# Optimization experiments

Measured on AMD Instinct MI355X. Metric: run time of the kernel, lower is better.

Reference implementation:

```python
import jax, jax.numpy as jnp
import numpy as np

N_NODES = 50000
N_EDGES = 200000
D = 128
LN_EPS = 1e-5


def _layer_norm(x, g, b):
    mu = jnp.mean(x, axis=-1, keepdims=True)
    var = jnp.mean(jnp.square(x - mu), axis=-1, keepdims=True)
    return (x - mu) * jax.lax.rsqrt(var + LN_EPS) * g + b


def _mlp(x, W1, b1, W2, b2, W3, b3, g, beta):
    # 2 hidden ReLU layers + linear output + LayerNorm (MeshGraphNets style)
    h = jax.nn.relu(x @ W1 + b1)
    h = jax.nn.relu(h @ W2 + b2)
    h = h @ W3 + b3
    return _layer_norm(h, g, beta)


def setup_inputs() -> dict:
    key = jax.random.key(0)
    ks = jax.random.split(key, 12)
    d = {}
    d["node_features"] = jax.random.normal(ks[0], (N_NODES, D), dtype=jnp.float32)
    d["edge_features"] = jax.random.normal(ks[1], (N_EDGES, D), dtype=jnp.float32)
    d["senders"] = jax.random.randint(ks[2], (N_EDGES,), 0, N_NODES, dtype=jnp.int32)
    d["receivers"] = jax.random.randint(ks[3], (N_EDGES,), 0, N_NODES, dtype=jnp.int32)
    def lin(k, fan_in, fan_out):
        return jax.random.normal(k, (fan_in, fan_out), dtype=jnp.float32) / np.sqrt(fan_in)
    # edge MLP: [3D] -> D -> D -> D
    d["We1"] = lin(ks[4], 3 * D, D); d["be1"] = jnp.zeros((D,), jnp.float32)
    d["We2"] = lin(ks[5], D, D);     d["be2"] = jnp.zeros((D,), jnp.float32)
    d["We3"] = lin(ks[6], D, D);     d["be3"] = jnp.zeros((D,), jnp.float32)
    d["ge"] = jnp.ones((D,), jnp.float32); d["bege"] = jnp.zeros((D,), jnp.float32)
    # node MLP: [2D] -> D -> D -> D
    d["Wn1"] = lin(ks[7], 2 * D, D); d["bn1"] = jnp.zeros((D,), jnp.float32)
    d["Wn2"] = lin(ks[8], D, D);     d["bn2"] = jnp.zeros((D,), jnp.float32)
    d["Wn3"] = lin(ks[9], D, D);     d["bn3"] = jnp.zeros((D,), jnp.float32)
    d["gn"] = jnp.ones((D,), jnp.float32); d["begn"] = jnp.zeros((D,), jnp.float32)
    return d


def reference(node_features, edge_features, senders, receivers,
              We1, be1, We2, be2, We3, be3, ge, bege,
              Wn1, bn1, Wn2, bn2, Wn3, bn3, gn, begn):
    num_nodes = node_features.shape[0]
    # --- edge update: gather sender/receiver feats, concat, edge MLP ---
    edge_in = jnp.concatenate(
        [node_features[senders], node_features[receivers], edge_features], axis=-1)  # [E, 3D]
    new_edge = _mlp(edge_in, We1, be1, We2, be2, We3, be3, ge, bege)  # [E, D]
    # --- node update: scatter-sum aggregate, concat, node MLP ---
    agg = jax.ops.segment_sum(new_edge, receivers, num_segments=num_nodes)  # [N, D]
    node_in = jnp.concatenate([node_features, agg], axis=-1)  # [N, 2D]
    new_node = _mlp(node_in, Wn1, bn1, Wn2, bn2, Wn3, bn3, gn, begn)
    # --- residuals ---
    new_node = new_node + node_features
    new_edge = new_edge + edge_features
    return new_node, new_edge
```

## Files before the change

kernel.cpp:

```cpp
#include <hip/hip_runtime.h>

#define NNODES 50000
#define NEDGES 200000
#define DD 128
#define LN_EPS 1e-5f
#define NTH 256

typedef __attribute__((ext_vector_type(8))) short bf16x8;
typedef __attribute__((ext_vector_type(4))) float f32x4;
typedef __attribute__((ext_vector_type(16))) float f32x16;

template<int N> struct ic { static constexpr int value = N; };

__device__ __forceinline__ unsigned short bfr(float f) {
    union { float f; unsigned u; } v; v.f = f;
    return (unsigned short)((v.u + 0x7fffu + ((v.u >> 16) & 1u)) >> 16);
}
__device__ __forceinline__ unsigned pk2(float a, float b) {
    return (unsigned)bfr(a) | ((unsigned)bfr(b) << 16);
}
__device__ __forceinline__ void gload_lds16(const void* g, void* l) {
    __builtin_amdgcn_global_load_lds(
        (const __attribute__((address_space(1))) void*)g,
        (__attribute__((address_space(3))) void*)l, 16, 0, 0);
}

__global__ __launch_bounds__(NTH)
void prepass(const float* __restrict__ We1, const float* __restrict__ We2,
             const float* __restrict__ We3, const float* __restrict__ Wn1,
             const float* __restrict__ Wn2, const float* __restrict__ Wn3,
             char* __restrict__ img_e, char* __restrict__ img_n,
             const float* __restrict__ nodef, const int* __restrict__ recv,
             uint4* __restrict__ nodb, int* __restrict__ cnt) {
    if (blockIdx.x < 72) {
        int tid = blockIdx.x * NTH + threadIdx.x;
        const float* W; char* dst; int q;
        if      (tid <  6144) { W = We1; dst = img_e;             q = tid;         }
        else if (tid <  8192) { W = We2; dst = img_e + 12 * 8192; q = tid - 6144;  }
        else if (tid < 10240) { W = We3; dst = img_e + 16 * 8192; q = tid - 8192;  }
        else if (tid < 14336) { W = Wn1; dst = img_n;             q = tid - 10240; }
        else if (tid < 16384) { W = Wn2; dst = img_n + 8 * 8192;  q = tid - 14336; }
        else if (tid < 18432) { W = Wn3; dst = img_n + 12 * 8192; q = tid - 16384; }
        else return;
        int c = q >> 9, rem = q & 511;
        int nt = rem >> 7, r2 = rem & 127, n32 = r2 >> 2, ks = r2 & 3;
        int n = nt * 32 + n32;
        int sx = (n32 + (n32 >> 2)) & 3;
        int k0 = c * 32 + ks * 8;
        unsigned short o[8];
        #pragma unroll
        for (int e = 0; e < 8; ++e)
            o[e] = bfr(W[(size_t)(k0 + e) * DD + n]);
        uint4 val;
        val.x = (unsigned)o[0] | ((unsigned)o[1] << 16);
        val.y = (unsigned)o[2] | ((unsigned)o[3] << 16);
        val.z = (unsigned)o[4] | ((unsigned)o[5] << 16);
        val.w = (unsigned)o[6] | ((unsigned)o[7] << 16);
        *(uint4*)(dst + (size_t)c * 8192 + nt * 2048 + n32 * 64 + ((ks ^ sx) << 4)) = val;
    } else {
        const int b = blockIdx.x - 72;
        const int tid0 = b * NTH + threadIdx.x;
        if (tid0 < NEDGES) atomicAdd(&cnt[recv[tid0]], 1);
        const int NG = NNODES * 16;
        for (int g = tid0; g < NG; g += 1024 * NTH) {
            f32x4 a = ((const f32x4*)nodef)[g * 2];
            f32x4 bb = ((const f32x4*)nodef)[g * 2 + 1];
            uint4 o;
            o.x = pk2(a[0], a[1]); o.y = pk2(a[2], a[3]);
            o.z = pk2(bb[0], bb[1]); o.w = pk2(bb[2], bb[3]);
            nodb[g] = o;
        }
    }
}

__global__ __launch_bounds__(NTH)
void csr_scan1(const int* __restrict__ cnt, int* __restrict__ part) {
    __shared__ int red[NTH];
    const int b = blockIdx.x, t = threadIdx.x;
    const int base = b * 196;
    int s = 0;
    for (int i = t; i < 196; i += NTH) {
        int idx = base + i;
        if (idx < NNODES) s += cnt[idx];
    }
    red[t] = s;
    __syncthreads();
    for (int d = NTH / 2; d > 0; d >>= 1) {
        if (t < d) red[t] += red[t + d];
        __syncthreads();
    }
    if (t == 0) part[b] = red[0];
}

__global__ __launch_bounds__(NTH)
void csr_scan2(const int* __restrict__ cnt, const int* __restrict__ part,
               int* __restrict__ off, int* __restrict__ cursor) {
    __shared__ int sp[NTH];
    const int t = threadIdx.x;
    sp[t] = part[t];
    __syncthreads();
    for (int d = 1; d < NTH; d <<= 1) {
        int v = (t >= d) ? sp[t - d] : 0;
        __syncthreads();
        sp[t] += v;
        __syncthreads();
    }
    int run = (t == 0) ? 0 : sp[t - 1];
    const int base = t * 196;
    for (int i = 0; i < 196; ++i) {
        int idx = base + i;
        if (idx < NNODES) { off[idx] = run; cursor[idx] = run; run += cnt[idx]; }
    }
    if (t == NTH - 1) off[NNODES] = NEDGES;
}

__global__ __launch_bounds__(NTH)
void aggregate(const unsigned* __restrict__ ybuf,
               const int* __restrict__ off,
               unsigned* __restrict__ aggb) {
    const int n = blockIdx.x * 4 + (threadIdx.x >> 6);
    const int l = threadIdx.x & 63;
    if (n >= NNODES) return;
    const int j0 = off[n], j1 = off[n + 1];
    float sx = 0.f, sy = 0.f;
    int j = j0;
    for (; j + 4 <= j1; j += 4) {
        unsigned v0 = ybuf[(size_t)j * 64 + l];
        unsigned v1 = ybuf[(size_t)(j + 1) * 64 + l];
        unsigned v2 = ybuf[(size_t)(j + 2) * 64 + l];
        unsigned v3 = ybuf[(size_t)(j + 3) * 64 + l];
        sx += __uint_as_float(v0 << 16) + __uint_as_float(v1 << 16)
            + __uint_as_float(v2 << 16) + __uint_as_float(v3 << 16);
        sy += __uint_as_float(v0 & 0xffff0000u) + __uint_as_float(v1 & 0xffff0000u)
            + __uint_as_float(v2 & 0xffff0000u) + __uint_as_float(v3 & 0xffff0000u);
    }
    for (; j < j1; ++j) {
        unsigned v = ybuf[(size_t)j * 64 + l];
        sx += __uint_as_float(v << 16);
        sy += __uint_as_float(v & 0xffff0000u);
    }
    aggb[(size_t)n * 64 + l] = pk2(sx, sy);
}

template<int MODE>
__global__ __launch_bounds__(NTH, 2)
void mgn_mfma(const float* __restrict__ nodef, const float* __restrict__ edgef,
              const unsigned short* __restrict__ nodb,
              const int* __restrict__ senders, const int* __restrict__ receivers,
              int* __restrict__ cursor,
              const char* __restrict__ img,
              const float* __restrict__ b1, const float* __restrict__ b2,
              const float* __restrict__ b3,
              const float* __restrict__ gamma, const float* __restrict__ beta,
              const unsigned short* __restrict__ aggb, unsigned* __restrict__ ybuf,
              float* __restrict__ outp)
{
    __shared__ char Wbuf[6 * 8192];
    __shared__ char Hb[4 * 8192];

    const int t  = threadIdx.x;
    const int w  = t >> 6;
    const int l  = t & 63;
    const int ln = l & 31;
    const int hi = l >> 5;
    const int row0 = blockIdx.x * 128;
    const int gm = row0 + w * 32 + ln;
    constexpr int NROWS = (MODE == 0) ? NEDGES : NNODES;
    constexpr int NK1   = (MODE == 0) ? 12 : 8;
    constexpr int NCH   = NK1 + 8;
    const int gmc = gm < NROWS ? gm : NROWS - 1;
    const int sxA = (ln + (ln >> 2)) & 3;
    const int sxH = ln & 15;

    int srow = 0, rrow = 0, prow = 0;
    if (MODE == 0) {
        srow = senders[gmc]; rrow = receivers[gmc];
        int pclaim = 0;
        if (hi == 0 && gm < NROWS) pclaim = atomicAdd(&cursor[rrow], 1);
        prow = __shfl(pclaim, ln);
    }

    const f32x16 fz = {0.f,0.f,0.f,0.f,0.f,0.f,0.f,0.f,
                       0.f,0.f,0.f,0.f,0.f,0.f,0.f,0.f};
    f32x16 acc[4];
    #pragma unroll
    for (int nt = 0; nt < 4; ++nt) acc[nt] = fz;

    bf16x8 bS[4][2];
    f32x4  fS[4][4];

    auto stageW = [&](int c) {
        const char* src = img + (size_t)c * 8192 + t * 16;
        char* dstl = Wbuf + (c % 6) * 8192 + t * 16;
        gload_lds16(src, dstl);
        gload_lds16(src + 4096, dstl + 4096);
    };

    auto loadBB = [&](auto CC, bf16x8* dst) {
        constexpr int c = decltype(CC)::value;
        const unsigned short* base;
        if constexpr (MODE == 0) {
            base = (c < 4) ? nodb + (size_t)srow * DD : nodb + (size_t)rrow * DD;
        } else {
            base = (c < 4) ? nodb + (size_t)gmc * DD : aggb + (size_t)gmc * DD;
        }
        const char* p = (const char*)base + (c & 3) * 64 + hi * 16;
        dst[0] = *(const bf16x8*)p;
        dst[1] = *(const bf16x8*)(p + 32);
    };

    auto loadBF = [&](auto CC, f32x4* dst) {
        constexpr int c = decltype(CC)::value;
        const float* p = edgef + (size_t)gmc * DD + (c & 3) * 32 + hi * 8;
        dst[0] = *(const f32x4*)p;
        dst[1] = *(const f32x4*)(p + 4);
        dst[2] = *(const f32x4*)(p + 16);
        dst[3] = *(const f32x4*)(p + 20);
    };

    auto cvtB = [&](const f32x4* br) {
        union { unsigned u[4]; bf16x8 v; } r;
        r.u[0] = pk2(br[0][0], br[0][1]);
        r.u[1] = pk2(br[0][2], br[0][3]);
        r.u[2] = pk2(br[1][0], br[1][1]);
        r.u[3] = pk2(br[1][2], br[1][3]);
        return r.v;
    };

    auto loadBH = [&](int ks, int kh) {
        const char* p = Hb + w * 8192 + ln * 256
                      + (((ks * 4 + kh * 2 + hi) ^ sxH) << 4);
        return *(const bf16x8*)p;
    };

    auto getB = [&](auto CC, int kh) -> bf16x8 {
        constexpr int c = decltype(CC)::value;
        if constexpr (c >= NK1) {
            return loadBH((c - NK1) & 3, kh);
        } else if constexpr (MODE == 0 && c >= 8) {
            return cvtB(&fS[c & 3][kh * 2]);
        } else {
            return bS[c & 3][kh];
        }
    };

    auto compute = [&](auto CC) {
        constexpr int c = decltype(CC)::value;
        const char* bp = Wbuf + (c % 6) * 8192 + ln * 64;
        #pragma unroll
        for (int kh = 0; kh < 2; ++kh) {
            bf16x8 b = getB(CC, kh);
            #pragma unroll
            for (int nt = 0; nt < 4; ++nt) {
                bf16x8 a = *(const bf16x8*)(bp + nt * 2048
                            + (((kh * 2 + hi) ^ sxA) << 4));
                acc[nt] = __builtin_amdgcn_mfma_f32_32x32x16_bf16(a, b, acc[nt], 0, 0, 0);
            }
        }
    };

    auto epiH = [&](const float* bias) {
        #pragma unroll
        for (int nt = 0; nt < 4; ++nt) {
            #pragma unroll
            for (int rq = 0; rq < 4; ++rq) {
                f32x4 bv = *(const f32x4*)(bias + nt * 32 + rq * 8 + hi * 4);
                unsigned short h[4];
                #pragma unroll
                for (int j = 0; j < 4; ++j)
                    h[j] = bfr(fmaxf(acc[nt][rq * 4 + j] + bv[j], 0.f));
                char* p = Hb + w * 8192 + ln * 256
                        + (((nt * 4 + rq) ^ sxH) << 4) + hi * 8;
                unsigned lo = (unsigned)h[0] | ((unsigned)h[1] << 16);
                unsigned hx = (unsigned)h[2] | ((unsigned)h[3] << 16);
                *(unsigned long long*)p =
                    (unsigned long long)lo | ((unsigned long long)hx << 32);
            }
            acc[nt] = fz;
        }
    };

    auto loadB = [&](auto CC) {
        constexpr int c = decltype(CC)::value;
        if constexpr (c < NK1) {
            if constexpr (MODE == 0 && c >= 8) loadBF(CC, fS[c & 3]);
            else                               loadBB(CC, bS[c & 3]);
        }
    };

#define PITER2(M, VM)                                                         \
    {                                                                         \
        __builtin_amdgcn_s_barrier();                                         \
        __builtin_amdgcn_sched_barrier(0);                                    \
        if constexpr (2*(M) + 4 < NCH) stageW(2*(M) + 4);                     \
        if constexpr (2*(M) + 5 < NCH) stageW(2*(M) + 5);                     \
        __builtin_amdgcn_sched_barrier(0);                                    \
        loadB(ic<2*(M) + 2>{});                                               \
        loadB(ic<2*(M) + 3>{});                                               \
        __builtin_amdgcn_sched_barrier(0);                                    \
        asm volatile("s_waitcnt vmcnt(" #VM ")" ::: "memory");                \
        __builtin_amdgcn_sched_barrier(0);                                    \
        compute(ic<2*(M)>{});                                                 \
        compute(ic<2*(M) + 1>{});                                             \
    }

    stageW(0);
    __builtin_amdgcn_sched_barrier(0);
    stageW(1);
    __builtin_amdgcn_sched_barrier(0);
    stageW(2);
    __builtin_amdgcn_sched_barrier(0);
    stageW(3);
    __builtin_amdgcn_sched_barrier(0);
    loadB(ic<0>{});
    loadB(ic<1>{});
    __builtin_amdgcn_sched_barrier(0);

    if constexpr (MODE == 0) {
        PITER2(0, 16)  PITER2(1, 20)  PITER2(2, 20)  PITER2(3, 24)
        PITER2(4, 28)  PITER2(5, 24)
        epiH(b1);
        PITER2(6, 16)  PITER2(7, 8)
        epiH(b2);
        PITER2(8, 4)   PITER2(9, 0)
    } else {
        PITER2(0, 16)  PITER2(1, 20)  PITER2(2, 20)  PITER2(3, 16)
        epiH(b1);
        PITER2(4, 12)  PITER2(5, 8)
        epiH(b2);
        PITER2(6, 4)   PITER2(7, 0)
    }
#undef PITER2

    float vsum = 0.f, vsq = 0.f;
    #pragma unroll
    for (int nt = 0; nt < 4; ++nt) {
        #pragma unroll
        for (int rq = 0; rq < 4; ++rq) {
            f32x4 bv = *(const f32x4*)(b3 + nt * 32 + rq * 8 + hi * 4);
            #pragma unroll
            for (int j = 0; j < 4; ++j) {
                float v = acc[nt][rq * 4 + j] + bv[j];
                acc[nt][rq * 4 + j] = v;
                vsum += v; vsq += v * v;
            }
        }
    }
    vsum += __shfl_xor(vsum, 32);
    vsq  += __shfl_xor(vsq, 32);
    const float mu = vsum * (1.f / DD);
    const float rs = rsqrtf(vsq * (1.f / DD) - mu * mu + LN_EPS);

    if (gm < NROWS) {
        const float* resid = ((MODE == 0) ? edgef : nodef) + (size_t)gm * DD;
        #pragma unroll
        for (int nt = 0; nt < 4; ++nt) {
            #pragma unroll
            for (int rq = 0; rq < 4; ++rq) {
                const int n0 = nt * 32 + rq * 8 + hi * 4;
                f32x4 gv = *(const f32x4*)(gamma + n0);
                f32x4 bv = *(const f32x4*)(beta + n0);
                f32x4 rv = *(const f32x4*)(resid + n0);
                float y[4];
                f32x4 o;
                #pragma unroll
                for (int j = 0; j < 4; ++j) {
                    y[j] = (acc[nt][rq * 4 + j] - mu) * rs * gv[j] + bv[j];
                    o[j] = y[j] + rv[j];
                }
                *(f32x4*)(outp + (size_t)gm * DD + n0) = o;
                if (MODE == 0) {
                    unsigned long long pkd =
                        (unsigned long long)pk2(y[0], y[1])
                      | ((unsigned long long)pk2(y[2], y[3]) << 32);
                    *(unsigned long long*)((char*)ybuf + (size_t)prow * 256 + n0 * 2) = pkd;
                }
            }
        }
    }
}

extern "C" void kernel_launch(void* const* d_in, const int* in_sizes, int n_in,
                              void* d_out, int out_size, void* d_ws, size_t ws_size,
                              hipStream_t stream) {
    const float* nodef = (const float*)d_in[0];
    const float* edgef = (const float*)d_in[1];
    const int* senders   = (const int*)d_in[2];
    const int* receivers = (const int*)d_in[3];
    const float* We1 = (const float*)d_in[4],  *be1 = (const float*)d_in[5];
    const float* We2 = (const float*)d_in[6],  *be2 = (const float*)d_in[7];
    const float* We3 = (const float*)d_in[8],  *be3 = (const float*)d_in[9];
    const float* ge  = (const float*)d_in[10], *bege = (const float*)d_in[11];
    const float* Wn1 = (const float*)d_in[12], *bn1 = (const float*)d_in[13];
    const float* Wn2 = (const float*)d_in[14], *bn2 = (const float*)d_in[15];
    const float* Wn3 = (const float*)d_in[16], *bn3 = (const float*)d_in[17];
    const float* gn  = (const float*)d_in[18], *begn = (const float*)d_in[19];

    float* out_node = (float*)d_out;
    float* out_edge = (float*)d_out + (size_t)NNODES * DD;

    char* ws = (char*)d_ws;
    size_t o = 0;
    unsigned short* aggb = (unsigned short*)(ws + o); o += (size_t)NNODES * 256;
    unsigned* ybuf = (unsigned*)(ws + o);             o += (size_t)NEDGES * 256;
    unsigned short* nodb = (unsigned short*)(ws + o); o += (size_t)NNODES * 256;
    char* img_e = ws + o;           o += 20 * 8192;
    char* img_n = ws + o;           o += 16 * 8192;
    int* cnt    = (int*)(ws + o);   o += NNODES * 4;
    int* cursor = (int*)(ws + o);   o += NNODES * 4;
    int* off    = (int*)(ws + o);   o += (NNODES + 4) * 4;
    int* part   = (int*)(ws + o);   o += NTH * 4;

    hipMemsetAsync(cnt, 0, NNODES * 4, stream);
    prepass<<<72 + 1024, NTH, 0, stream>>>(We1, We2, We3, Wn1, Wn2, Wn3,
                                           img_e, img_n,
                                           nodef, receivers, (uint4*)nodb, cnt);
    csr_scan1<<<NTH, NTH, 0, stream>>>(cnt, part);
    csr_scan2<<<1, NTH, 0, stream>>>(cnt, part, off, cursor);

    mgn_mfma<0><<<dim3((NEDGES + 127) / 128), dim3(NTH), 0, stream>>>(
        nodef, edgef, nodb, senders, receivers, cursor, img_e,
        be1, be2, be3, ge, bege, aggb, ybuf, out_edge);

    aggregate<<<(NNODES + 3) / 4, NTH, 0, stream>>>(ybuf, off, (unsigned*)aggb);

    mgn_mfma<1><<<dim3((NNODES + 127) / 128), dim3(NTH), 0, stream>>>(
        nodef, edgef, nodb, senders, receivers, cursor, img_n,
        bn1, bn2, bn3, gn, begn, aggb, ybuf, out_node);
}
```

Measured before the change: 302.8 us.

## Precompute per-node first-layer projections and gather them per edge

The sender and receiver parts of the first edge-MLP layer are linear in the node features, so a new kernel computes node·W_s and node·W_r once per node into a bf16 buffer P. The edge kernel gathers the two 128-wide projections, adds them to seed the accumulator, and runs only the edge-feature part of layer 1. This cuts the edge layer-1 MFMA work from 384 to 128 input channels and replaces two 256-byte node gathers with two 256-byte projection gathers. The cost is an extra kernel, a 25 MB projection buffer, and an extra bf16 rounding of the projections before the bias and ReLU.

```diff
diff --git a/kernel.cpp b/kernel.cpp
--- a/kernel.cpp
+++ b/kernel.cpp
@@ -73,6 +73,74 @@
     }
 }
 
+__global__ __launch_bounds__(NTH, 2)
+void proj_nodes(const unsigned short* __restrict__ nodb,
+                const char* __restrict__ img_e,
+                unsigned short* __restrict__ P) {
+    __shared__ char Wb[8 * 8192];
+    const int t = threadIdx.x;
+    const int w = t >> 6;
+    const int l = t & 63;
+    const int ln = l & 31;
+    const int hi = l >> 5;
+    const int p  = w >> 1;
+    const int gm = blockIdx.x * 64 + (w & 1) * 32 + ln;
+    const int gmc = gm < NNODES ? gm : NNODES - 1;
+    const int sxA = (ln + (ln >> 2)) & 3;
+
+    #pragma unroll
+    for (int c = 0; c < 8; ++c) {
+        const char* src = img_e + (size_t)c * 8192 + t * 16;
+        char* d = Wb + c * 8192 + t * 16;
+        gload_lds16(src, d);
+        gload_lds16(src + 4096, d + 4096);
+    }
+    bf16x8 b[4][2];
+    #pragma unroll
+    for (int c = 0; c < 4; ++c) {
+        const char* q = (const char*)(nodb + (size_t)gmc * DD) + c * 64 + hi * 16;
+        b[c][0] = *(const bf16x8*)q;
+        b[c][1] = *(const bf16x8*)(q + 32);
+    }
+    asm volatile("s_waitcnt vmcnt(0)" ::: "memory");
+    __builtin_amdgcn_s_barrier();
+
+    const f32x16 fz = {0.f,0.f,0.f,0.f,0.f,0.f,0.f,0.f,
+                       0.f,0.f,0.f,0.f,0.f,0.f,0.f,0.f};
+    f32x16 acc[4];
+    #pragma unroll
+    for (int nt = 0; nt < 4; ++nt) acc[nt] = fz;
+
+    #pragma unroll
+    for (int c = 0; c < 4; ++c) {
+        const char* bp = Wb + (p * 4 + c) * 8192 + ln * 64;
+        #pragma unroll
+        for (int kh = 0; kh < 2; ++kh) {
+            #pragma unroll
+            for (int nt = 0; nt < 4; ++nt) {
+                bf16x8 a = *(const bf16x8*)(bp + nt * 2048
+                            + (((kh * 2 + hi) ^ sxA) << 4));
+                acc[nt] = __builtin_amdgcn_mfma_f32_32x32x16_bf16(a, b[c][kh], acc[nt], 0, 0, 0);
+            }
+        }
+    }
+    if (gm < NNODES) {
+        unsigned short* out = P + (size_t)gm * 256 + p * 128 + hi * 64;
+        #pragma unroll
+        for (int nt = 0; nt < 4; ++nt) {
+            #pragma unroll
+            for (int rp = 0; rp < 2; ++rp) {
+                uint4 v;
+                v.x = pk2(acc[nt][rp * 8 + 0], acc[nt][rp * 8 + 1]);
+                v.y = pk2(acc[nt][rp * 8 + 2], acc[nt][rp * 8 + 3]);
+                v.z = pk2(acc[nt][rp * 8 + 4], acc[nt][rp * 8 + 5]);
+                v.w = pk2(acc[nt][rp * 8 + 6], acc[nt][rp * 8 + 7]);
+                *(uint4*)(out + nt * 16 + rp * 8) = v;
+            }
+        }
+    }
+}
+
 __global__ __launch_bounds__(NTH)
 void csr_scan1(const int* __restrict__ cnt, int* __restrict__ part) {
     __shared__ int red[NTH];
@@ -146,6 +214,7 @@
 __global__ __launch_bounds__(NTH, 2)
 void mgn_mfma(const float* __restrict__ nodef, const float* __restrict__ edgef,
               const unsigned short* __restrict__ nodb,
+              const unsigned short* __restrict__ P,
               const int* __restrict__ senders, const int* __restrict__ receivers,
               int* __restrict__ cursor,
               const char* __restrict__ img,
@@ -166,7 +235,7 @@
     const int row0 = blockIdx.x * 128;
     const int gm = row0 + w * 32 + ln;
     constexpr int NROWS = (MODE == 0) ? NEDGES : NNODES;
-    constexpr int NK1   = (MODE == 0) ? 12 : 8;
+    constexpr int NK1   = (MODE == 0) ? 4 : 8;
     constexpr int NCH   = NK1 + 8;
     const int gmc = gm < NROWS ? gm : NROWS - 1;
     const int sxA = (ln + (ln >> 2)) & 3;
@@ -183,8 +252,30 @@
     const f32x16 fz = {0.f,0.f,0.f,0.f,0.f,0.f,0.f,0.f,
                        0.f,0.f,0.f,0.f,0.f,0.f,0.f,0.f};
     f32x16 acc[4];
-    #pragma unroll
-    for (int nt = 0; nt < 4; ++nt) acc[nt] = fz;
+
+    if constexpr (MODE == 0) {
+        const unsigned short* Ps = P + (size_t)srow * 256 + hi * 64;
+        const unsigned short* Pr = P + (size_t)rrow * 256 + 128 + hi * 64;
+        bf16x8 pv[16];
+        #pragma unroll
+        for (int k = 0; k < 8; ++k) pv[k]     = *(const bf16x8*)(Ps + k * 8);
+        #pragma unroll
+        for (int k = 0; k < 8; ++k) pv[8 + k] = *(const bf16x8*)(Pr + k * 8);
+        #pragma unroll
+        for (int k = 0; k < 8; ++k) {
+            const int nt = k >> 1, rb = (k & 1) * 8;
+            #pragma unroll
+            for (int e = 0; e < 8; ++e) {
+                float vs = __uint_as_float((unsigned)(unsigned short)pv[k][e] << 16);
+                float vr = __uint_as_float((unsigned)(unsigned short)pv[8 + k][e] << 16);
+                acc[nt][rb + e] = vs + vr;
+            }
+        }
+    } else {
+        #pragma unroll
+        for (int nt = 0; nt < 4; ++nt) acc[nt] = fz;
+    }
+    __builtin_amdgcn_sched_barrier(0);
 
     bf16x8 bS[4][2];
     f32x4  fS[4][4];
@@ -198,12 +289,8 @@
 
     auto loadBB = [&](auto CC, bf16x8* dst) {
         constexpr int c = decltype(CC)::value;
-        const unsigned short* base;
-        if constexpr (MODE == 0) {
-            base = (c < 4) ? nodb + (size_t)srow * DD : nodb + (size_t)rrow * DD;
-        } else {
-            base = (c < 4) ? nodb + (size_t)gmc * DD : aggb + (size_t)gmc * DD;
-        }
+        const unsigned short* base =
+            (c < 4) ? nodb + (size_t)gmc * DD : aggb + (size_t)gmc * DD;
         const char* p = (const char*)base + (c & 3) * 64 + hi * 16;
         dst[0] = *(const bf16x8*)p;
         dst[1] = *(const bf16x8*)(p + 32);
@@ -237,7 +324,7 @@
         constexpr int c = decltype(CC)::value;
         if constexpr (c >= NK1) {
             return loadBH((c - NK1) & 3, kh);
-        } else if constexpr (MODE == 0 && c >= 8) {
+        } else if constexpr (MODE == 0) {
             return cvtB(&fS[c & 3][kh * 2]);
         } else {
             return bS[c & 3][kh];
@@ -283,8 +370,8 @@
     auto loadB = [&](auto CC) {
         constexpr int c = decltype(CC)::value;
         if constexpr (c < NK1) {
-            if constexpr (MODE == 0 && c >= 8) loadBF(CC, fS[c & 3]);
-            else                               loadBB(CC, bS[c & 3]);
+            if constexpr (MODE == 0) loadBF(CC, fS[c & 3]);
+            else                     loadBB(CC, bS[c & 3]);
         }
     };
 
@@ -317,12 +404,11 @@
     __builtin_amdgcn_sched_barrier(0);
 
     if constexpr (MODE == 0) {
-        PITER2(0, 16)  PITER2(1, 20)  PITER2(2, 20)  PITER2(3, 24)
-        PITER2(4, 28)  PITER2(5, 24)
+        PITER2(0, 12)  PITER2(1, 4)
         epiH(b1);
-        PITER2(6, 16)  PITER2(7, 8)
+        PITER2(2, 8)   PITER2(3, 8)
         epiH(b2);
-        PITER2(8, 4)   PITER2(9, 0)
+        PITER2(4, 4)   PITER2(5, 0)
     } else {
         PITER2(0, 16)  PITER2(1, 20)  PITER2(2, 20)  PITER2(3, 16)
         epiH(b1);
@@ -404,6 +490,7 @@
     unsigned short* aggb = (unsigned short*)(ws + o); o += (size_t)NNODES * 256;
     unsigned* ybuf = (unsigned*)(ws + o);             o += (size_t)NEDGES * 256;
     unsigned short* nodb = (unsigned short*)(ws + o); o += (size_t)NNODES * 256;
+    unsigned short* P = (unsigned short*)(ws + o);    o += (size_t)NNODES * 512;
     char* img_e = ws + o;           o += 20 * 8192;
     char* img_n = ws + o;           o += 16 * 8192;
     int* cnt    = (int*)(ws + o);   o += NNODES * 4;
@@ -415,16 +502,17 @@
     prepass<<<72 + 1024, NTH, 0, stream>>>(We1, We2, We3, Wn1, Wn2, Wn3,
                                            img_e, img_n,
                                            nodef, receivers, (uint4*)nodb, cnt);
+    proj_nodes<<<(NNODES + 63) / 64, NTH, 0, stream>>>(nodb, img_e, P);
     csr_scan1<<<NTH, NTH, 0, stream>>>(cnt, part);
     csr_scan2<<<1, NTH, 0, stream>>>(cnt, part, off, cursor);
 
     mgn_mfma<0><<<dim3((NEDGES + 127) / 128), dim3(NTH), 0, stream>>>(
-        nodef, edgef, nodb, senders, receivers, cursor, img_e,
+        nodef, edgef, nodb, P, senders, receivers, cursor, img_e + 8 * 8192,
         be1, be2, be3, ge, bege, aggb, ybuf, out_edge);
 
     aggregate<<<(NNODES + 3) / 4, NTH, 0, stream>>>(ybuf, off, (unsigned*)aggb);
 
     mgn_mfma<1><<<dim3((NNODES + 127) / 128), dim3(NTH), 0, stream>>>(
-        nodef, edgef, nodb, senders, receivers, cursor, img_n,
+        nodef, edgef, nodb, P, senders, receivers, cursor, img_n,
         bn1, bn2, bn3, gn, begn, aggb, ybuf, out_node);
 }
```

After: 323.0 us. +6.7%, slower.
